# Performance work log

Hardware: AMD Instinct MI355X
Metric: run time of the kernel (lower is better)

The kernel has to match this reference:

```python
import jax, jax.numpy as jnp
import numpy as np

N_SAMPLE, N_ATOMS, N_TOKENS, N_CHAINS = 4, 8192, 1024, 8
AF3_THR = 1.1  # af3_clash_threshold
COUNT_THR = 100  # total_clash > 100
REL_THR = 0.5    # relative_clash > 0.5


def setup_inputs() -> dict:
    key = jax.random.key(0)
    k1, = jax.random.split(key, 1)
    # coords spread out a bit so clashes are sparse-ish but nonzero
    pred_coordinate = jax.random.normal(k1, (N_SAMPLE, N_ATOMS, 3), dtype=jnp.float32) * 5.0
    # balanced sorted chain assignment per token: guarantees all ids 0..N_CHAINS-1 present
    asym_id = ((jnp.arange(N_TOKENS) * N_CHAINS) // N_TOKENS).astype(jnp.int32)
    # monotone atoms -> tokens map (N_ATOMS // N_TOKENS atoms per token)
    atom_to_token_idx = (jnp.arange(N_ATOMS) // (N_ATOMS // N_TOKENS)).astype(jnp.int32)
    return {
        "pred_coordinate": pred_coordinate,
        "asym_id": asym_id,
        "atom_to_token_idx": atom_to_token_idx,
    }


def reference(pred_coordinate, asym_id, atom_to_token_idx):
    # Per-atom chain id, then one-hot chain membership M: [N_atoms, N_chains]
    atom_chain = asym_id[atom_to_token_idx]
    M = jax.nn.one_hot(atom_chain, N_CHAINS, dtype=pred_coordinate.dtype)
    n_per_chain = M.sum(axis=0)  # [C] atoms per chain

    # Squared pairwise distances via gram expansion (avoids [S,N,N,3] diff tensor)
    sq = jnp.sum(pred_coordinate * pred_coordinate, axis=-1)          # [S, N]
    gram = jnp.einsum('snd,smd->snm', pred_coordinate, pred_coordinate)  # [S, N, N]
    d2 = sq[:, :, None] + sq[:, None, :] - 2.0 * gram                 # [S, N, N]

    # dist < thr  <=>  d2 < thr^2 (both non-negative)
    clash = (d2 < AF3_THR * AF3_THR).astype(pred_coordinate.dtype)

    # counts[s, a, b] = #{(i in chain a, j in chain b) : clash}; two small GEMMs
    counts = jnp.einsum('snm,na,mb->sab', clash, M, M)  # [S, C, C]

    # original only fills strict off-diagonal pairs (i < j, mirrored); diagonal stays 0
    off = 1.0 - jnp.eye(N_CHAINS, dtype=counts.dtype)
    total = counts * off
    min_n = jnp.minimum(n_per_chain[:, None], n_per_chain[None, :])
    rel = total / min_n

    af3_clash_details = jnp.stack([total, rel], axis=-1)  # [S, C, C, 2]
    has_af3_clash = (total > COUNT_THR) | (rel > REL_THR)  # [S, C, C] bool
    return has_af3_clash, af3_clash_details
```

## Files before the change

kernel.cpp:

```cpp
#include <hip/hip_runtime.h>

#define NS 4
#define NA 8192
#define NTOK 1024
#define NC 8
#define THREADS 256
#define JSLOTS 4
#define JPB (THREADS * JSLOTS)
#define TI 128
#define NJB (NA / JPB)
#define NIB (NA / TI)


__global__ __launch_bounds__(THREADS, 8)
void clash_kernel(const float* __restrict__ coords, const int* __restrict__ asym,
                  const int* __restrict__ a2t, int* __restrict__ counts) {
  __shared__ float4 tile[TI];
  __shared__ int tchain[TI];
  __shared__ int red[NC * NC];

  const int tid = threadIdx.x;
  const int ib = blockIdx.x, jb = blockIdx.y, s = blockIdx.z;
  if (tid < NC * NC) red[tid] = 0;

  const float* __restrict__ base = coords + (size_t)s * NA * 3;
  const float THR2 = 1.21f;

  float xj[JSLOTS], yj[JSLOTS], zj[JSLOTS], tj[JSLOTS];
  int bj[JSLOTS];
#pragma unroll
  for (int u = 0; u < JSLOTS; ++u) {
    int j = jb * JPB + u * THREADS + tid;
    float x = base[3 * j + 0], y = base[3 * j + 1], z = base[3 * j + 2];
    xj[u] = x; yj[u] = y; zj[u] = z;
    tj[u] = x * x + y * y + z * z;
    bj[u] = asym[a2t[j]];
  }
  if (tid < TI) {
    int i = ib * TI + tid;
    float x = base[3 * i + 0], y = base[3 * i + 1], z = base[3 * i + 2];
    tile[tid] = make_float4(2.0f * x, 2.0f * y, 2.0f * z, THR2 - (x * x + y * y + z * z));
    tchain[tid] = asym[a2t[i]];
  }
  __syncthreads();

  int uni_a = __syncthreads_and(tchain[tid & (TI - 1)] == tchain[0]);

  if (uni_a) {
    int acc[JSLOTS];
#pragma unroll
    for (int u = 0; u < JSLOTS; ++u) acc[u] = 0;
#pragma unroll 8
    for (int t = 0; t < TI; ++t) {
      float4 ci = tile[t];
#pragma unroll
      for (int u = 0; u < JSLOTS; ++u) {
        float d = fmaf(ci.x, xj[u], fmaf(ci.y, yj[u], fmaf(ci.z, zj[u], ci.w)));
        acc[u] += (d > tj[u]);
      }
    }
    const int A = tchain[0];
#pragma unroll
    for (int u = 0; u < JSLOTS; ++u) {
      int v = acc[u];
      int b0 = __builtin_amdgcn_readfirstlane(bj[u]);
      if (__all(bj[u] == b0)) {
#pragma unroll
        for (int m = 32; m >= 1; m >>= 1) v += __shfl_xor(v, m, 64);
        if ((tid & 63) == 0 && v) atomicAdd(&red[A * NC + b0], v);
      } else if (v) {
        atomicAdd(&red[A * NC + bj[u]], v);
      }
    }
  } else {
    for (int t = 0; t < TI; ++t) {
      int a = tchain[t];
      float4 ci = tile[t];
#pragma unroll
      for (int u = 0; u < JSLOTS; ++u) {
        float d = fmaf(ci.x, xj[u], fmaf(ci.y, yj[u], fmaf(ci.z, zj[u], ci.w)));
        if (d > tj[u]) atomicAdd(&red[a * NC + bj[u]], 1);
      }
    }
  }

  __syncthreads();
  if (tid < NC * NC) {
    int v = red[tid];
    if (v) atomicAdd(&counts[s * NC * NC + tid], v);
  }
}

__global__ __launch_bounds__(THREADS)
void finalize_kernel(const int* __restrict__ asym, const int* __restrict__ counts,
                     float* __restrict__ out) {
  __shared__ int hist[NC];
  int tid = threadIdx.x;
  if (tid < NC) hist[tid] = 0;
  __syncthreads();
  for (int t = tid; t < NTOK; t += THREADS) atomicAdd(&hist[asym[t]], NA / NTOK);
  __syncthreads();

  int c = counts[tid];
  int a = (tid >> 3) & 7, b = tid & 7;
  float total = (a == b) ? 0.0f : (float)c;
  float minn = (float)min(hist[a], hist[b]);
  float rel = total / minn;
  out[tid] = ((total > 100.0f) || (rel > 0.5f)) ? 1.0f : 0.0f;
  out[256 + 2 * tid + 0] = total;
  out[256 + 2 * tid + 1] = rel;
}

extern "C" void kernel_launch(void* const* d_in, const int* in_sizes, int n_in,
                              void* d_out, int out_size, void* d_ws, size_t ws_size,
                              hipStream_t stream) {
  const float* coords = (const float*)d_in[0];
  const int* asym = (const int*)d_in[1];
  const int* a2t = (const int*)d_in[2];
  float* out = (float*)d_out;

  int* counts = (int*)d_ws;

  hipMemsetAsync(counts, 0, NS * NC * NC * sizeof(int), stream);
  clash_kernel<<<dim3(NIB, NJB, NS), THREADS, 0, stream>>>(coords, asym, a2t, counts);
  finalize_kernel<<<1, THREADS, 0, stream>>>(asym, counts, out);
}
```

Measured before the change: 92.06 us.

## Precompute staged i-coordinates and chain ids in setup kernel, read tiles from global

Adds a setup kernel that builds per-atom float4 values (2x, 2y, 2z, thr² minus |x|²) and per-atom chain ids, and zeroes the counts, replacing the memset. The clash kernel then reads i-atom data straight from global memory with a uniform address instead of staging it in shared memory, and gets chain ids without the double indirection. This removes LDS staging and the gather chain, at the cost of an extra launch and uniform global loads inside the inner loop.

```diff
diff --git a/kernel.cpp b/kernel.cpp
--- a/kernel.cpp
+++ b/kernel.cpp
@@ -12,10 +12,22 @@
 #define NIB (NA / TI)
 
 
+__global__ __launch_bounds__(THREADS)
+void setup_kernel(const float* __restrict__ coords, const int* __restrict__ asym,
+                  const int* __restrict__ a2t, float4* __restrict__ staged,
+                  int* __restrict__ chain, int* __restrict__ counts) {
+  const float THR2 = 1.21f;
+  int idx = blockIdx.x * THREADS + threadIdx.x;
+  float x = coords[3 * idx + 0], y = coords[3 * idx + 1], z = coords[3 * idx + 2];
+  staged[idx] = make_float4(2.0f * x, 2.0f * y, 2.0f * z,
+                            THR2 - (x * x + y * y + z * z));
+  if (idx < NA) chain[idx] = asym[a2t[idx]];
+  if (idx < NS * NC * NC) counts[idx] = 0;
+}
+
 __global__ __launch_bounds__(THREADS, 8)
-void clash_kernel(const float* __restrict__ coords, const int* __restrict__ asym,
-                  const int* __restrict__ a2t, int* __restrict__ counts) {
-  __shared__ float4 tile[TI];
+void clash_kernel(const float* __restrict__ coords, const float4* __restrict__ staged,
+                  const int* __restrict__ chain, int* __restrict__ counts) {
   __shared__ int tchain[TI];
   __shared__ int red[NC * NC];
 
@@ -24,7 +36,6 @@
   if (tid < NC * NC) red[tid] = 0;
 
   const float* __restrict__ base = coords + (size_t)s * NA * 3;
-  const float THR2 = 1.21f;
 
   float xj[JSLOTS], yj[JSLOTS], zj[JSLOTS], tj[JSLOTS];
   int bj[JSLOTS];
@@ -34,17 +45,14 @@
     float x = base[3 * j + 0], y = base[3 * j + 1], z = base[3 * j + 2];
     xj[u] = x; yj[u] = y; zj[u] = z;
     tj[u] = x * x + y * y + z * z;
-    bj[u] = asym[a2t[j]];
+    bj[u] = chain[j];
   }
-  if (tid < TI) {
-    int i = ib * TI + tid;
-    float x = base[3 * i + 0], y = base[3 * i + 1], z = base[3 * i + 2];
-    tile[tid] = make_float4(2.0f * x, 2.0f * y, 2.0f * z, THR2 - (x * x + y * y + z * z));
-    tchain[tid] = asym[a2t[i]];
-  }
+  if (tid < TI) tchain[tid] = chain[ib * TI + tid];
   __syncthreads();
 
   int uni_a = __syncthreads_and(tchain[tid & (TI - 1)] == tchain[0]);
+
+  const float4* __restrict__ tg = staged + (size_t)s * NA + ib * TI;
 
   if (uni_a) {
     int acc[JSLOTS];
@@ -52,7 +60,7 @@
     for (int u = 0; u < JSLOTS; ++u) acc[u] = 0;
 #pragma unroll 8
     for (int t = 0; t < TI; ++t) {
-      float4 ci = tile[t];
+      float4 ci = tg[t];
 #pragma unroll
       for (int u = 0; u < JSLOTS; ++u) {
         float d = fmaf(ci.x, xj[u], fmaf(ci.y, yj[u], fmaf(ci.z, zj[u], ci.w)));
@@ -75,7 +83,7 @@
   } else {
     for (int t = 0; t < TI; ++t) {
       int a = tchain[t];
-      float4 ci = tile[t];
+      float4 ci = tg[t];
 #pragma unroll
       for (int u = 0; u < JSLOTS; ++u) {
         float d = fmaf(ci.x, xj[u], fmaf(ci.y, yj[u], fmaf(ci.z, zj[u], ci.w)));
@@ -119,9 +127,12 @@
   const int* a2t = (const int*)d_in[2];
   float* out = (float*)d_out;
 
-  int* counts = (int*)d_ws;
+  float4* staged = (float4*)d_ws;
+  int* chain = (int*)(staged + NS * NA);
+  int* counts = chain + NA;
 
-  hipMemsetAsync(counts, 0, NS * NC * NC * sizeof(int), stream);
-  clash_kernel<<<dim3(NIB, NJB, NS), THREADS, 0, stream>>>(coords, asym, a2t, counts);
+  setup_kernel<<<dim3(NS * NA / THREADS), THREADS, 0, stream>>>(coords, asym, a2t,
+                                                                staged, chain, counts);
+  clash_kernel<<<dim3(NIB, NJB, NS), THREADS, 0, stream>>>(coords, staged, chain, counts);
   finalize_kernel<<<1, THREADS, 0, stream>>>(asym, counts, out);
 }
```

New measurement: 96.16 us. 1.04x slower.
